# Kernel tuning notes

Hardware: AMD Instinct MI355X
Metric: run time of the kernel (lower is better)

Reference implementation:

```python
import jax, jax.numpy as jnp
import numpy as np

EMBED_DIM = 1024
NUM_HEADS = 16
HEAD_DIM = EMBED_DIM // NUM_HEADS
B, S = 4, 1024
EPS = 1e-5
NEG = -1e9


def layer_norm(h, gamma, beta):
    mu = jnp.mean(h, axis=-1, keepdims=True)
    var = jnp.mean(jnp.square(h - mu), axis=-1, keepdims=True)
    return (h - mu) * jax.lax.rsqrt(var + EPS) * gamma + beta


def setup_inputs() -> dict:
    key = jax.random.key(0)
    ks = jax.random.split(key, 8)
    scale = 1.0 / np.sqrt(EMBED_DIM)
    x = jax.random.normal(ks[0], (B, S, EMBED_DIM), dtype=jnp.float32)
    mask = jax.random.randint(ks[1], (B, S, S), 0, 2).astype(jnp.bool_)
    Wq = jax.random.uniform(ks[2], (EMBED_DIM, EMBED_DIM), jnp.float32, -scale, scale)
    bq = jax.random.uniform(ks[3], (EMBED_DIM,), jnp.float32, -scale, scale)
    Wk = jax.random.uniform(ks[4], (EMBED_DIM, EMBED_DIM), jnp.float32, -scale, scale)
    bk = jax.random.uniform(ks[5], (EMBED_DIM,), jnp.float32, -scale, scale)
    gq = jnp.ones((EMBED_DIM,), jnp.float32)
    bq_n = jnp.zeros((EMBED_DIM,), jnp.float32)
    gk = jnp.ones((EMBED_DIM,), jnp.float32)
    bk_n = jnp.zeros((EMBED_DIM,), jnp.float32)
    return {"x": x, "mask": mask, "Wq": Wq, "bq": bq, "Wk": Wk, "bk": bk,
            "gq": gq, "bq_n": bq_n, "gk": gk, "bk_n": bk_n}


def reference(x, mask, Wq, bq, Wk, bk, gq, bq_n, gk, bk_n):
    b, s, _ = x.shape
    # proj -> LayerNorm -> ReLU, split heads: [B,S,H,D]
    Q = jax.nn.relu(layer_norm(x @ Wq + bq, gq, bq_n)).reshape(b, s, NUM_HEADS, HEAD_DIM)
    K = jax.nn.relu(layer_norm(x @ Wk + bk, gk, bk_n)).reshape(b, s, NUM_HEADS, HEAD_DIM)
    # scores [B,H,S,S]
    scores = jnp.einsum('bqhd,bkhd->bhqk', Q, K) / np.sqrt(HEAD_DIM).astype(np.float32)
    # symmetric masking: mask applied along keys, then (via transpose trick) along queries
    m = (mask | jnp.swapaxes(mask, -1, -2))[:, None, :, :]
    scores = jnp.where(m, NEG, scores)
    attn = jax.nn.softmax(scores, axis=-1)
    return attn.mean(axis=1)  # [B,S,S]
```

## Files before the change

### kernel.cpp

```cpp
#include <hip/hip_runtime.h>
#include <hip/hip_bf16.h>

#define B_ 4
#define S_ 1024
#define E_ 1024
#define H_ 16
#define D_ 64

typedef __attribute__((ext_vector_type(8))) short short8;
typedef __attribute__((ext_vector_type(4))) float f32x4;

static __device__ __forceinline__ unsigned short f2bf(float x) {
  unsigned int u = __float_as_uint(x);
  unsigned int r = u + 0x7fffu + ((u >> 16) & 1u);
  return (unsigned short)(r >> 16);
}
static __device__ __forceinline__ float bf2f(unsigned short b) {
  return __uint_as_float((unsigned int)b << 16);
}

#define GL2LDS16(g, l)                                                            \
  __builtin_amdgcn_global_load_lds(                                               \
      (const __attribute__((address_space(1))) unsigned int*)(g),                 \
      (__attribute__((address_space(3))) unsigned int*)(l), 16, 0, 0)

#define QSCALE 0.18033688011112042f
#define SCLAMP 115.41560327111707f

static __device__ __forceinline__ float dpp_red16(float v) {
  v += __int_as_float(__builtin_amdgcn_update_dpp(0, __float_as_int(v), 0xB1, 0xF, 0xF, true));
  v += __int_as_float(__builtin_amdgcn_update_dpp(0, __float_as_int(v), 0x4E, 0xF, 0xF, true));
  v += __int_as_float(__builtin_amdgcn_update_dpp(0, __float_as_int(v), 0x141, 0xF, 0xF, true));
  v += __int_as_float(__builtin_amdgcn_update_dpp(0, __float_as_int(v), 0x140, 0xF, 0xF, true));
  return v;
}

__global__ __launch_bounds__(256) void prep_kernel(const int* __restrict__ mask,
                                                   const float* __restrict__ x,
                                                   const float* __restrict__ Wq,
                                                   const float* __restrict__ Wk,
                                                   unsigned char* __restrict__ msym,
                                                   unsigned short* __restrict__ xbf,
                                                   unsigned short* __restrict__ Wt) {
  __shared__ __align__(16) char u_lds[32 * 33 * 4];
  const int blk = blockIdx.x;
  const int tid = threadIdx.x;
  if (blk < 4096) {
    int (*T)[33] = (int(*)[33])u_lds;
    const int b = blk >> 10;
    const int rest = blk & 1023;
    const int i0 = (rest >> 5) << 5;
    const int j0 = (rest & 31) << 5;
    const int ii = tid >> 3;
    const int jj4 = (tid & 7) << 2;
    const size_t bO = (size_t)b * S_ * S_;
    const int4 m2 = *(const int4*)&mask[bO + (size_t)(j0 + ii) * S_ + i0 + jj4];
    T[ii][jj4 + 0] = m2.x; T[ii][jj4 + 1] = m2.y; T[ii][jj4 + 2] = m2.z; T[ii][jj4 + 3] = m2.w;
    __syncthreads();
    const int4 m1 = *(const int4*)&mask[bO + (size_t)(i0 + ii) * S_ + j0 + jj4];
    uchar4 o;
    o.x = ((m1.x != 0) || (T[jj4 + 0][ii] != 0)) ? 1 : 0;
    o.y = ((m1.y != 0) || (T[jj4 + 1][ii] != 0)) ? 1 : 0;
    o.z = ((m1.z != 0) || (T[jj4 + 2][ii] != 0)) ? 1 : 0;
    o.w = ((m1.w != 0) || (T[jj4 + 3][ii] != 0)) ? 1 : 0;
    *(uchar4*)&msym[bO + (size_t)(i0 + ii) * S_ + j0 + jj4] = o;
  } else if (blk < 6144) {
    const size_t i = ((size_t)(blk - 4096) * 256 + tid) * 8;
    const float4 a = *(const float4*)(x + i);
    const float4 b = *(const float4*)(x + i + 4);
    const ushort4 p0 = {f2bf(a.x), f2bf(a.y), f2bf(a.z), f2bf(a.w)};
    const ushort4 p1 = {f2bf(b.x), f2bf(b.y), f2bf(b.z), f2bf(b.w)};
    *(ushort4*)(xbf + i) = p0;
    *(ushort4*)(xbf + i + 4) = p1;
  } else {
    unsigned short (*T2)[36] = (unsigned short(*)[36])u_lds;
    const int wblk = blk - 6144;
    const int mat = wblk >> 10;
    const int kt = (wblk >> 5) & 31, ntb = wblk & 31;
    const float* W = mat ? Wk : Wq;
    const int r = tid >> 3, c4 = (tid & 7) << 2;
    const float4 v = *(const float4*)&W[(size_t)(kt * 32 + r) * 1024 + ntb * 32 + c4];
    T2[r][c4 + 0] = f2bf(v.x); T2[r][c4 + 1] = f2bf(v.y);
    T2[r][c4 + 2] = f2bf(v.z); T2[r][c4 + 3] = f2bf(v.w);
    __syncthreads();
    const ushort4 o = {T2[c4 + 0][r], T2[c4 + 1][r], T2[c4 + 2][r], T2[c4 + 3][r]};
    *(ushort4*)&Wt[(size_t)(mat * 1024 + ntb * 32 + r) * 1024 + kt * 32 + c4] = o;
  }
}

__global__ __launch_bounds__(256) void gemm_mfma_kernel(const unsigned short* __restrict__ Abf,
                                                        const unsigned short* __restrict__ Wt,
                                                        unsigned short* __restrict__ P,
                                                        int nstride) {
  __shared__ __align__(16) unsigned short As[128 * 64];
  __shared__ __align__(16) unsigned short Bs[128 * 64];
  const int tid = threadIdx.x;
  const int m0 = (blockIdx.x & 31) << 7;
  const int n0 = (blockIdx.x >> 5) << 7;
  const int wave = tid >> 6, lane = tid & 63;
  const int ln15 = lane & 15, rg = lane >> 4;
  const int wm = (wave & 1) << 6;
  const int wn = (wave >> 1) << 6;
  const int sr = tid >> 3;
  const int sc = (tid & 7) << 3;
  const unsigned short* gA = Abf + (size_t)(m0 + sr) * 1024 + sc;
  const unsigned short* gB = Wt + (size_t)(n0 + sr) * 1024 + sc;
  unsigned short* lA = As + tid * 8;
  unsigned short* lB = Bs + tid * 8;
  f32x4 acc[4][4];
#pragma unroll
  for (int i = 0; i < 4; ++i)
#pragma unroll
    for (int j = 0; j < 4; ++j) acc[i][j] = (f32x4){0.0f, 0.0f, 0.0f, 0.0f};

  const unsigned short* pa = As + (wm + ln15) * 64 + rg * 8;
  const unsigned short* pb = Bs + (wn + ln15) * 64 + rg * 8;
  for (int k0 = 0; k0 < E_; k0 += 64) {
#pragma unroll
    for (int j = 0; j < 4; ++j) {
      GL2LDS16(gA + k0 + (size_t)(j * 32) * 1024, lA + j * 2048);
      GL2LDS16(gB + k0 + (size_t)(j * 32) * 1024, lB + j * 2048);
    }
    __syncthreads();
#pragma unroll
    for (int kk = 0; kk < 2; ++kk) {
      short8 af[4], bfr[4];
#pragma unroll
      for (int i = 0; i < 4; ++i) af[i] = *(const short8*)(pa + i * 16 * 64 + kk * 32);
#pragma unroll
      for (int j = 0; j < 4; ++j) bfr[j] = *(const short8*)(pb + j * 16 * 64 + kk * 32);
#pragma unroll
      for (int i = 0; i < 4; ++i)
#pragma unroll
        for (int j = 0; j < 4; ++j)
          acc[i][j] = __builtin_amdgcn_mfma_f32_16x16x32_bf16(af[i], bfr[j], acc[i][j], 0, 0, 0);
    }
    __syncthreads();
  }
#pragma unroll
  for (int i = 0; i < 4; ++i)
#pragma unroll
    for (int j = 0; j < 4; ++j)
#pragma unroll
      for (int r = 0; r < 4; ++r) {
        const int row = m0 + wm + i * 16 + rg * 4 + r;
        const int col = n0 + wn + j * 16 + ln15;
        P[(size_t)row * nstride + col] = f2bf(acc[i][j][r]);
      }
}

__device__ __forceinline__ void ln_body(const unsigned short* p, const float* bias,
                                        const float* gamma, const float* beta,
                                        unsigned short* obf, int b, int s, int tid) {
  const ushort4 pv = *(const ushort4*)(p + tid * 4);
  float4 v = {bf2f(pv.x), bf2f(pv.y), bf2f(pv.z), bf2f(pv.w)};
  const float4 bb = ((const float4*)bias)[tid];
  v.x += bb.x; v.y += bb.y; v.z += bb.z; v.w += bb.w;
  float sum = v.x + v.y + v.z + v.w;
  float s2 = v.x * v.x + v.y * v.y + v.z * v.z + v.w * v.w;
#pragma unroll
  for (int off = 32; off >= 1; off >>= 1) {
    sum += __shfl_xor(sum, off);
    s2 += __shfl_xor(s2, off);
  }
  __shared__ float red[2][4];
  const int wave = tid >> 6, lane = tid & 63;
  if (lane == 0) { red[0][wave] = sum; red[1][wave] = s2; }
  __syncthreads();
  sum = red[0][0] + red[0][1] + red[0][2] + red[0][3];
  s2 = red[1][0] + red[1][1] + red[1][2] + red[1][3];
  const float mu = sum * (1.0f / E_);
  const float var = s2 * (1.0f / E_) - mu * mu;
  const float r = rsqrtf(var + 1e-5f);
  const float4 g = ((const float4*)gamma)[tid];
  const float4 bt = ((const float4*)beta)[tid];
  const float o0 = fmaxf((v.x - mu) * r * g.x + bt.x, 0.0f);
  const float o1 = fmaxf((v.y - mu) * r * g.y + bt.y, 0.0f);
  const float o2 = fmaxf((v.z - mu) * r * g.z + bt.z, 0.0f);
  const float o3 = fmaxf((v.w - mu) * r * g.w + bt.w, 0.0f);
  const int h = tid >> 4;
  const int d = (tid & 15) << 2;
  const ushort4 ob = {f2bf(o0), f2bf(o1), f2bf(o2), f2bf(o3)};
  *(ushort4*)&obf[((size_t)(b * H_ + h) * S_ + s) * D_ + d] = ob;
}

__global__ __launch_bounds__(256) void ln_relu_bf_kernel(const unsigned short* __restrict__ P,
                                                         int rowstride, int coloff,
                                                         const float* __restrict__ bias,
                                                         const float* __restrict__ gamma,
                                                         const float* __restrict__ beta,
                                                         unsigned short* __restrict__ obf) {
  const int row = blockIdx.x;
  ln_body(P + (size_t)row * rowstride + coloff, bias, gamma, beta, obf,
          row >> 10, row & 1023, threadIdx.x);
}

__global__ __launch_bounds__(256) void ln2_kernel(const unsigned short* __restrict__ P2,
                                                  const float* __restrict__ bq,
                                                  const float* __restrict__ gq,
                                                  const float* __restrict__ bqn,
                                                  const float* __restrict__ bk,
                                                  const float* __restrict__ gk,
                                                  const float* __restrict__ bkn,
                                                  unsigned short* __restrict__ Qbf,
                                                  unsigned short* __restrict__ Kbf) {
  const int blk = blockIdx.x;
  const int sel = blk >> 12;
  const int row = blk & 4095;
  ln_body(P2 + (size_t)row * 2048 + sel * 1024,
          sel ? bk : bq, sel ? gk : gq, sel ? bkn : bqn,
          sel ? Kbf : Qbf, row >> 10, row & 1023, threadIdx.x);
}

__global__ __launch_bounds__(1024, 4) void attn13_kernel(const unsigned short* __restrict__ Qbf,
                                                         const unsigned short* __restrict__ Kbf,
                                                         const unsigned char* __restrict__ msym,
                                                         float* __restrict__ out) {
  __shared__ __align__(16) float l_lds[2][16][20];
  const int tid = threadIdx.x;
  const int wave = tid >> 6, lane = tid & 63;
  const int ln15 = lane & 15, rg = lane >> 4;
  const int b = blockIdx.x & 3;
  const int q0 = (blockIdx.x >> 2) << 4;
  const unsigned short* Kb = Kbf + (size_t)b * H_ * S_ * D_;
  const unsigned short* Qb = Qbf + (size_t)b * H_ * S_ * D_;

  unsigned int mbits = 0;
#pragma unroll
  for (int hf = 0; hf < 2; ++hf)
#pragma unroll
    for (int jt = 0; jt < 2; ++jt)
#pragma unroll
      for (int r = 0; r < 4; ++r)
        mbits |= (msym[((size_t)b * S_ + q0 + rg * 4 + r) * S_ + hf * 512 + wave * 32 + jt * 16 + ln15]
                      ? 1u : 0u) << (hf * 8 + jt * 4 + r);
  float mf[2][2][4];
#pragma unroll
  for (int hf = 0; hf < 2; ++hf)
#pragma unroll
    for (int jt = 0; jt < 2; ++jt)
#pragma unroll
      for (int r = 0; r < 4; ++r)
        mf[hf][jt][r] = ((mbits >> (hf * 8 + jt * 4 + r)) & 1u) ? 0.0f : 1.0f;

  const unsigned short* kb0 = Kb + (size_t)(wave * 32 + ln15) * D_ + rg * 8;
  const unsigned short* kb1 = kb0 + (size_t)512 * D_;
  const unsigned short* qp = Qb + (size_t)(q0 + ln15) * D_ + rg * 8;

  float o[2][2][4] = {};
  float ef[2][2][4];
  float la[4];

#pragma unroll 1
  for (int h = 0; h < 16; ++h) {
    const short8 a0 = *(const short8*)qp;
    const short8 a1 = *(const short8*)(qp + 32);
    const short8 k00a = *(const short8*)(kb0);
    const short8 k00b = *(const short8*)(kb0 + 32);
    const short8 k01a = *(const short8*)(kb0 + 1024);
    const short8 k01b = *(const short8*)(kb0 + 1056);
    const short8 k10a = *(const short8*)(kb1);
    const short8 k10b = *(const short8*)(kb1 + 32);
    const short8 k11a = *(const short8*)(kb1 + 1024);
    const short8 k11b = *(const short8*)(kb1 + 1056);
    la[0] = la[1] = la[2] = la[3] = 0.0f;
#pragma unroll
    for (int hf = 0; hf < 2; ++hf) {
#pragma unroll
      for (int jt = 0; jt < 2; ++jt) {
        const short8 b0 = hf ? (jt ? k11a : k10a) : (jt ? k01a : k00a);
        const short8 b1 = hf ? (jt ? k11b : k10b) : (jt ? k01b : k00b);
        f32x4 cc = {0.0f, 0.0f, 0.0f, 0.0f};
        cc = __builtin_amdgcn_mfma_f32_16x16x32_bf16(a0, b0, cc, 0, 0, 0);
        cc = __builtin_amdgcn_mfma_f32_16x16x32_bf16(a1, b1, cc, 0, 0, 0);
#pragma unroll
        for (int r = 0; r < 4; ++r) {
          const float sv = fminf(cc[r] * QSCALE, SCLAMP);
          const float ev = __builtin_amdgcn_exp2f(sv) * mf[hf][jt][r];
          ef[hf][jt][r] = ev;
          la[r] += ev;
        }
      }
    }
#pragma unroll
    for (int r = 0; r < 4; ++r) la[r] = dpp_red16(la[r]);
    if (ln15 == 0) *(f32x4*)&l_lds[h & 1][wave][rg * 4] = (f32x4){la[0], la[1], la[2], la[3]};
    __syncthreads();
    const f32x4 pw = *(const f32x4*)&l_lds[h & 1][ln15][rg * 4];
#pragma unroll
    for (int r = 0; r < 4; ++r) {
      const float li = __builtin_amdgcn_rcpf(dpp_red16(pw[r]));
#pragma unroll
      for (int hf = 0; hf < 2; ++hf)
#pragma unroll
        for (int jt = 0; jt < 2; ++jt) o[hf][jt][r] += ef[hf][jt][r] * li;
    }
    qp += (size_t)S_ * D_;
    kb0 += (size_t)S_ * D_;
    kb1 += (size_t)S_ * D_;
  }
#pragma unroll
  for (int hf = 0; hf < 2; ++hf)
#pragma unroll
    for (int jt = 0; jt < 2; ++jt)
#pragma unroll
      for (int r = 0; r < 4; ++r)
        out[((size_t)b * S_ + q0 + rg * 4 + r) * S_ + hf * 512 + wave * 32 + jt * 16 + ln15] =
            o[hf][jt][r] * 0.0625f;
}

extern "C" void kernel_launch(void* const* d_in, const int* in_sizes, int n_in,
                              void* d_out, int out_size, void* d_ws, size_t ws_size,
                              hipStream_t stream) {
  const float* x = (const float*)d_in[0];
  const int* mask = (const int*)d_in[1];
  const float* Wq = (const float*)d_in[2];
  const float* bq = (const float*)d_in[3];
  const float* Wk = (const float*)d_in[4];
  const float* bk = (const float*)d_in[5];
  const float* gq = (const float*)d_in[6];
  const float* bq_n = (const float*)d_in[7];
  const float* gk = (const float*)d_in[8];
  const float* bk_n = (const float*)d_in[9];
  float* out = (float*)d_out;

  char* ws = (char*)d_ws;
  const size_t MB = 1024 * 1024;

  if (ws_size >= 40 * MB) {
    unsigned short* P2 = (unsigned short*)ws;
    unsigned short* xbf = (unsigned short*)(ws + 16 * MB);
    unsigned short* Kbf = (unsigned short*)(ws + 16 * MB);
    unsigned short* Wt = (unsigned short*)(ws + 24 * MB);
    unsigned short* Qbf = (unsigned short*)(ws + 28 * MB);
    unsigned char* msym = (unsigned char*)(ws + 36 * MB);

    prep_kernel<<<8192, 256, 0, stream>>>(mask, x, Wq, Wk, msym, xbf, Wt);
    gemm_mfma_kernel<<<512, 256, 0, stream>>>(xbf, Wt, P2, 2048);
    ln2_kernel<<<8192, 256, 0, stream>>>(P2, bq, gq, bq_n, bk, gk, bk_n, Qbf, Kbf);
    attn13_kernel<<<256, 1024, 0, stream>>>(Qbf, Kbf, msym, out);
  } else {
    unsigned short* P = (unsigned short*)ws;
    unsigned short* xbf = (unsigned short*)(ws + 8 * MB);
    unsigned short* Kbf = (unsigned short*)(ws + 8 * MB);
    unsigned short* Wt = (unsigned short*)(ws + 16 * MB);
    unsigned short* Qbf = (unsigned short*)(ws + 20 * MB);
    unsigned char* msym = (unsigned char*)(ws + 28 * MB);

    prep_kernel<<<8192, 256, 0, stream>>>(mask, x, Wq, Wk, msym, xbf, Wt);
    gemm_mfma_kernel<<<256, 256, 0, stream>>>(xbf, Wt, P, 1024);
    ln_relu_bf_kernel<<<4096, 256, 0, stream>>>(P, 1024, 0, bq, gq, bq_n, Qbf);
    gemm_mfma_kernel<<<256, 256, 0, stream>>>(xbf, Wt + (size_t)1024 * 1024, P, 1024);
    ln_relu_bf_kernel<<<4096, 256, 0, stream>>>(P, 1024, 0, bk, gk, bk_n, Kbf);
    attn13_kernel<<<256, 1024, 0, stream>>>(Qbf, Kbf, msym, out);
  }
}
```

Baseline: 219.9 us.

## Split attention into row-sum pass and output pass with finer tiling

Replaces the single attention kernel, which covered full key rows per block and synchronised once per head, with two kernels. The first computes per-(batch, head, query) softmax denominators and stores their reciprocals in a workspace buffer. The second tiles over query and key blocks and recomputes the scores to accumulate the head-averaged probabilities. This removes per-head block barriers and the large 1024-thread blocks and gives more, smaller blocks, at the cost of computing the QK^T product and exp twice and an extra launch.

```diff
diff --git a/kernel.cpp b/kernel.cpp
--- a/kernel.cpp
+++ b/kernel.cpp
@@ -212,101 +212,109 @@
           sel ? Kbf : Qbf, row >> 10, row & 1023, threadIdx.x);
 }
 
-__global__ __launch_bounds__(1024, 4) void attn13_kernel(const unsigned short* __restrict__ Qbf,
-                                                         const unsigned short* __restrict__ Kbf,
-                                                         const unsigned char* __restrict__ msym,
-                                                         float* __restrict__ out) {
-  __shared__ __align__(16) float l_lds[2][16][20];
+
+__global__ __launch_bounds__(256, 4) void attn_l_kernel(const unsigned short* __restrict__ Qbf,
+                                                        const unsigned short* __restrict__ Kbf,
+                                                        const unsigned char* __restrict__ msym,
+                                                        float* __restrict__ linv) {
   const int tid = threadIdx.x;
   const int wave = tid >> 6, lane = tid & 63;
   const int ln15 = lane & 15, rg = lane >> 4;
-  const int b = blockIdx.x & 3;
-  const int q0 = (blockIdx.x >> 2) << 4;
-  const unsigned short* Kb = Kbf + (size_t)b * H_ * S_ * D_;
-  const unsigned short* Qb = Qbf + (size_t)b * H_ * S_ * D_;
-
-  unsigned int mbits = 0;
-#pragma unroll
-  for (int hf = 0; hf < 2; ++hf)
-#pragma unroll
-    for (int jt = 0; jt < 2; ++jt)
-#pragma unroll
-      for (int r = 0; r < 4; ++r)
-        mbits |= (msym[((size_t)b * S_ + q0 + rg * 4 + r) * S_ + hf * 512 + wave * 32 + jt * 16 + ln15]
-                      ? 1u : 0u) << (hf * 8 + jt * 4 + r);
-  float mf[2][2][4];
-#pragma unroll
-  for (int hf = 0; hf < 2; ++hf)
-#pragma unroll
-    for (int jt = 0; jt < 2; ++jt)
-#pragma unroll
-      for (int r = 0; r < 4; ++r)
-        mf[hf][jt][r] = ((mbits >> (hf * 8 + jt * 4 + r)) & 1u) ? 0.0f : 1.0f;
-
-  const unsigned short* kb0 = Kb + (size_t)(wave * 32 + ln15) * D_ + rg * 8;
-  const unsigned short* kb1 = kb0 + (size_t)512 * D_;
-  const unsigned short* qp = Qb + (size_t)(q0 + ln15) * D_ + rg * 8;
-
-  float o[2][2][4] = {};
-  float ef[2][2][4];
-  float la[4];
-
+  const int blk = blockIdx.x;
+  const int b = blk >> 8;
+  const int h = (blk >> 4) & 15;
+  const int qt = blk & 15;
+  const int q0 = qt * 64 + wave * 16;
+  const size_t bh = (size_t)(b * H_ + h);
+  const unsigned short* qp = Qbf + (bh * S_ + q0 + ln15) * D_ + rg * 8;
+  const short8 a0 = *(const short8*)qp;
+  const short8 a1 = *(const short8*)(qp + 32);
+  const unsigned short* kp = Kbf + (bh * S_ + ln15) * D_ + rg * 8;
+  const unsigned char* mrow = msym + ((size_t)b * S_ + q0 + rg * 4) * S_ + ln15;
+  float la[4] = {0.0f, 0.0f, 0.0f, 0.0f};
+#pragma unroll 2
+  for (int c = 0; c < 16; ++c) {
+#pragma unroll
+    for (int t = 0; t < 4; ++t) {
+      const int kbase = c * 64 + t * 16;
+      const unsigned short* kf = kp + (size_t)kbase * D_;
+      const short8 b0 = *(const short8*)kf;
+      const short8 b1 = *(const short8*)(kf + 32);
+      f32x4 cc = {0.0f, 0.0f, 0.0f, 0.0f};
+      cc = __builtin_amdgcn_mfma_f32_16x16x32_bf16(a0, b0, cc, 0, 0, 0);
+      cc = __builtin_amdgcn_mfma_f32_16x16x32_bf16(a1, b1, cc, 0, 0, 0);
+#pragma unroll
+      for (int r = 0; r < 4; ++r) {
+        const unsigned char m = mrow[(size_t)r * S_ + kbase];
+        const float sv = fminf(cc[r] * QSCALE, SCLAMP);
+        const float ev = __builtin_amdgcn_exp2f(sv);
+        la[r] += m ? 0.0f : ev;
+      }
+    }
+  }
+#pragma unroll
+  for (int r = 0; r < 4; ++r) la[r] = dpp_red16(la[r]);
+  if (ln15 == 0) {
+    const f32x4 wv = {__builtin_amdgcn_rcpf(la[0]), __builtin_amdgcn_rcpf(la[1]),
+                      __builtin_amdgcn_rcpf(la[2]), __builtin_amdgcn_rcpf(la[3])};
+    *(f32x4*)&linv[bh * S_ + q0 + rg * 4] = wv;
+  }
+}
+
+__global__ __launch_bounds__(256, 4) void attn_o_kernel(const unsigned short* __restrict__ Qbf,
+                                                        const unsigned short* __restrict__ Kbf,
+                                                        const unsigned char* __restrict__ msym,
+                                                        const float* __restrict__ linv,
+                                                        float* __restrict__ out) {
+  const int tid = threadIdx.x;
+  const int wave = tid >> 6, lane = tid & 63;
+  const int ln15 = lane & 15, rg = lane >> 4;
+  const int blk = blockIdx.x;
+  const int b = blk >> 8;
+  const int qt = (blk >> 4) & 15;
+  const int kt = blk & 15;
+  const int q0 = qt * 64 + wave * 16;
+  const int k0 = kt * 64;
+  float mf[4][4];
+#pragma unroll
+  for (int t = 0; t < 4; ++t)
+#pragma unroll
+    for (int r = 0; r < 4; ++r)
+      mf[t][r] = msym[((size_t)b * S_ + q0 + rg * 4 + r) * S_ + k0 + t * 16 + ln15] ? 0.0f : 1.0f;
+
+  const unsigned short* qp = Qbf + ((size_t)(b * H_) * S_ + q0 + ln15) * D_ + rg * 8;
+  const unsigned short* kp = Kbf + ((size_t)(b * H_) * S_ + k0 + ln15) * D_ + rg * 8;
+  const float* lp = linv + (size_t)(b * H_) * S_ + q0 + rg * 4;
+  const size_t HD = (size_t)S_ * D_;
+
+  float o[4][4] = {};
 #pragma unroll 1
   for (int h = 0; h < 16; ++h) {
     const short8 a0 = *(const short8*)qp;
     const short8 a1 = *(const short8*)(qp + 32);
-    const short8 k00a = *(const short8*)(kb0);
-    const short8 k00b = *(const short8*)(kb0 + 32);
-    const short8 k01a = *(const short8*)(kb0 + 1024);
-    const short8 k01b = *(const short8*)(kb0 + 1056);
-    const short8 k10a = *(const short8*)(kb1);
-    const short8 k10b = *(const short8*)(kb1 + 32);
-    const short8 k11a = *(const short8*)(kb1 + 1024);
-    const short8 k11b = *(const short8*)(kb1 + 1056);
-    la[0] = la[1] = la[2] = la[3] = 0.0f;
-#pragma unroll
-    for (int hf = 0; hf < 2; ++hf) {
-#pragma unroll
-      for (int jt = 0; jt < 2; ++jt) {
-        const short8 b0 = hf ? (jt ? k11a : k10a) : (jt ? k01a : k00a);
-        const short8 b1 = hf ? (jt ? k11b : k10b) : (jt ? k01b : k00b);
-        f32x4 cc = {0.0f, 0.0f, 0.0f, 0.0f};
-        cc = __builtin_amdgcn_mfma_f32_16x16x32_bf16(a0, b0, cc, 0, 0, 0);
-        cc = __builtin_amdgcn_mfma_f32_16x16x32_bf16(a1, b1, cc, 0, 0, 0);
-#pragma unroll
-        for (int r = 0; r < 4; ++r) {
-          const float sv = fminf(cc[r] * QSCALE, SCLAMP);
-          const float ev = __builtin_amdgcn_exp2f(sv) * mf[hf][jt][r];
-          ef[hf][jt][r] = ev;
-          la[r] += ev;
-        }
+    const f32x4 li = *(const f32x4*)lp;
+#pragma unroll
+    for (int t = 0; t < 4; ++t) {
+      const unsigned short* kf = kp + (size_t)(t * 16) * D_;
+      const short8 b0 = *(const short8*)kf;
+      const short8 b1 = *(const short8*)(kf + 32);
+      f32x4 cc = {0.0f, 0.0f, 0.0f, 0.0f};
+      cc = __builtin_amdgcn_mfma_f32_16x16x32_bf16(a0, b0, cc, 0, 0, 0);
+      cc = __builtin_amdgcn_mfma_f32_16x16x32_bf16(a1, b1, cc, 0, 0, 0);
+#pragma unroll
+      for (int r = 0; r < 4; ++r) {
+        const float sv = fminf(cc[r] * QSCALE, SCLAMP);
+        const float ev = __builtin_amdgcn_exp2f(sv) * mf[t][r];
+        o[t][r] += ev * li[r];
       }
     }
-#pragma unroll
-    for (int r = 0; r < 4; ++r) la[r] = dpp_red16(la[r]);
-    if (ln15 == 0) *(f32x4*)&l_lds[h & 1][wave][rg * 4] = (f32x4){la[0], la[1], la[2], la[3]};
-    __syncthreads();
-    const f32x4 pw = *(const f32x4*)&l_lds[h & 1][ln15][rg * 4];
-#pragma unroll
-    for (int r = 0; r < 4; ++r) {
-      const float li = __builtin_amdgcn_rcpf(dpp_red16(pw[r]));
-#pragma unroll
-      for (int hf = 0; hf < 2; ++hf)
-#pragma unroll
-        for (int jt = 0; jt < 2; ++jt) o[hf][jt][r] += ef[hf][jt][r] * li;
-    }
-    qp += (size_t)S_ * D_;
-    kb0 += (size_t)S_ * D_;
-    kb1 += (size_t)S_ * D_;
-  }
-#pragma unroll
-  for (int hf = 0; hf < 2; ++hf)
-#pragma unroll
-    for (int jt = 0; jt < 2; ++jt)
-#pragma unroll
-      for (int r = 0; r < 4; ++r)
-        out[((size_t)b * S_ + q0 + rg * 4 + r) * S_ + hf * 512 + wave * 32 + jt * 16 + ln15] =
-            o[hf][jt][r] * 0.0625f;
+    qp += HD; kp += HD; lp += S_;
+  }
+#pragma unroll
+  for (int t = 0; t < 4; ++t)
+#pragma unroll
+    for (int r = 0; r < 4; ++r)
+      out[((size_t)b * S_ + q0 + rg * 4 + r) * S_ + k0 + t * 16 + ln15] = o[t][r] * 0.0625f;
 }
 
 extern "C" void kernel_launch(void* const* d_in, const int* in_sizes, int n_in,
@@ -334,11 +342,13 @@
     unsigned short* Wt = (unsigned short*)(ws + 24 * MB);
     unsigned short* Qbf = (unsigned short*)(ws + 28 * MB);
     unsigned char* msym = (unsigned char*)(ws + 36 * MB);
+    float* linv = (float*)(ws + 24 * MB);
 
     prep_kernel<<<8192, 256, 0, stream>>>(mask, x, Wq, Wk, msym, xbf, Wt);
     gemm_mfma_kernel<<<512, 256, 0, stream>>>(xbf, Wt, P2, 2048);
     ln2_kernel<<<8192, 256, 0, stream>>>(P2, bq, gq, bq_n, bk, gk, bk_n, Qbf, Kbf);
-    attn13_kernel<<<256, 1024, 0, stream>>>(Qbf, Kbf, msym, out);
+    attn_l_kernel<<<1024, 256, 0, stream>>>(Qbf, Kbf, msym, linv);
+    attn_o_kernel<<<1024, 256, 0, stream>>>(Qbf, Kbf, msym, linv, out);
   } else {
     unsigned short* P = (unsigned short*)ws;
     unsigned short* xbf = (unsigned short*)(ws + 8 * MB);
@@ -346,12 +356,14 @@
     unsigned short* Wt = (unsigned short*)(ws + 16 * MB);
     unsigned short* Qbf = (unsigned short*)(ws + 20 * MB);
     unsigned char* msym = (unsigned char*)(ws + 28 * MB);
+    float* linv = (float*)(ws + 16 * MB);
 
     prep_kernel<<<8192, 256, 0, stream>>>(mask, x, Wq, Wk, msym, xbf, Wt);
     gemm_mfma_kernel<<<256, 256, 0, stream>>>(xbf, Wt, P, 1024);
     ln_relu_bf_kernel<<<4096, 256, 0, stream>>>(P, 1024, 0, bq, gq, bq_n, Qbf);
     gemm_mfma_kernel<<<256, 256, 0, stream>>>(xbf, Wt + (size_t)1024 * 1024, P, 1024);
     ln_relu_bf_kernel<<<4096, 256, 0, stream>>>(P, 1024, 0, bk, gk, bk_n, Kbf);
-    attn13_kernel<<<256, 1024, 0, stream>>>(Qbf, Kbf, msym, out);
-  }
-}
+    attn_l_kernel<<<1024, 256, 0, stream>>>(Qbf, Kbf, msym, linv);
+    attn_o_kernel<<<1024, 256, 0, stream>>>(Qbf, Kbf, msym, linv, out);
+  }
+}
```

Measured after the change: 280.4 us. 1.27x slower.
